# Optimization experiments

Measured on AMD Instinct MI355X. Metric: run time of the kernel, lower is better.

## Reference

```python
import jax, jax.numpy as jnp
import numpy as np

B, T, D = 4, 2048, 1024
F = 4 * D  # Config.RWKV_INTERMIDATE_SIZE * hidden_dim
LN_EPS = 1e-3  # keras LayerNormalization default epsilon


def layer_norm(x, g, b, eps=LN_EPS):
    mu = jnp.mean(x, axis=-1, keepdims=True)
    var = jnp.mean(jnp.square(x - mu), axis=-1, keepdims=True)
    return (x - mu) * jax.lax.rsqrt(var + eps) * g + b


def setup_inputs() -> dict:
    ks = jax.random.split(jax.random.key(0), 24)
    g = lambda k, shape: (jax.random.normal(k, shape, jnp.float32)
                          * np.sqrt(2.0 / sum(shape)))  # ~glorot
    return {
        "x": jax.random.normal(ks[0], (B, T, D), jnp.float32),
        "s_cm": jnp.zeros((B, D), jnp.float32),
        "s_tm": jnp.zeros((B, D), jnp.float32),
        "s_num": jnp.zeros((B, D), jnp.float32),
        "s_den": jnp.zeros((B, D), jnp.float32),
        "s_q": jnp.zeros((B, D), jnp.float32),
        "ln1_g": jnp.ones((D,), jnp.float32),
        "ln1_b": jnp.zeros((D,), jnp.float32),
        "ln2_g": jnp.ones((D,), jnp.float32),
        "ln2_b": jnp.zeros((D,), jnp.float32),
        "tm_mix_k": jax.random.uniform(ks[1], (D,), jnp.float32, 0.0, 2.0 / D),
        "tm_mix_v": jax.random.uniform(ks[2], (D,), jnp.float32, 0.0, 2.0 / D),
        "tm_mix_r": jax.random.uniform(ks[3], (D,), jnp.float32, 0.0, (2.0 / D) ** 0.5),
        "tm_kw": g(ks[4], (D, D)),
        "tm_vw": g(ks[5], (D, D)),
        "tm_rw": g(ks[6], (D, D)),
        "time_decay": jax.random.uniform(ks[7], (D,), jnp.float32, 0.0, 0.1),
        "time_first": jax.random.uniform(ks[8], (D,), jnp.float32, 0.0, 0.05),
        "out_w": g(ks[9], (D, D)),
        "cm_mix_k": jax.random.uniform(ks[10], (D,), jnp.float32, 0.0, 2.0 / D),
        "cm_mix_r": jax.random.uniform(ks[11], (D,), jnp.float32, 0.0, 2.0 / D),
        "cm_kw": g(ks[12], (D, F)),
        "cm_vw": g(ks[13], (F, D)),
        "cm_rw": g(ks[14], (D, D)),
    }


def _shift(h, s):
    # token shift: prepend last-token state, drop last timestep
    return jnp.concatenate([s[:, None, :], h[:, :-1, :]], axis=1)


def reference(x, s_cm, s_tm, s_num, s_den, s_q,
              ln1_g, ln1_b, ln2_g, ln2_b,
              tm_mix_k, tm_mix_v, tm_mix_r, tm_kw, tm_vw, tm_rw,
              time_decay, time_first, out_w,
              cm_mix_k, cm_mix_r, cm_kw, cm_vw, cm_rw):
    # ---- time mixing ----
    h = layer_norm(x, ln1_g, ln1_b)  # [B,T,D]
    hs = _shift(h, s_tm)
    xk = h * tm_mix_k + hs * (1.0 - tm_mix_k)
    xv = h * tm_mix_v + hs * (1.0 - tm_mix_v)
    xr = h * tm_mix_r + hs * (1.0 - tm_mix_r)
    k = xk @ tm_kw  # [B,T,D]
    v = xv @ tm_vw
    r = jax.nn.sigmoid(xr @ tm_rw)
    w = -jnp.exp(time_decay)  # [D]

    def step(carry, kv):
        num, den, q = carry
        kt, vt = kv  # [B,D]
        mo = jnp.maximum(q, kt + time_first)
        e1 = jnp.exp(q - mo)
        e2 = jnp.exp(kt + time_first - mo)
        out = (e1 * num + e2 * vt) / (e1 * den + e2)
        ms = jnp.maximum(q + w, kt)
        e1s = jnp.exp(q + w - ms)
        e2s = jnp.exp(kt - ms)
        return (e1s * num + e2s * vt, e1s * den + e2s, ms), out

    (num, den, q), wkv = jax.lax.scan(
        step, (s_num, s_den, s_q),
        (k.transpose(1, 0, 2), v.transpose(1, 0, 2)))
    wkv = wkv.transpose(1, 0, 2)  # [B,T,D]
    x = x + (r * wkv) @ out_w

    # ---- channel mixing ----
    h2 = layer_norm(x, ln2_g, ln2_b)
    hs2 = _shift(h2, s_cm)
    xk2 = h2 * cm_mix_k + hs2 * (1.0 - cm_mix_k)
    xr2 = h2 * cm_mix_r + hs2 * (1.0 - cm_mix_r)
    kv = jnp.square(jax.nn.relu(xk2 @ cm_kw)) @ cm_vw  # [B,T,F] -> [B,T,D]
    x = x + jax.nn.sigmoid(xr2 @ cm_rw) * kv

    # new state: (cm_inputs, tm_inputs, num, den, q)
    return x, h2[:, -1], h[:, -1], num, den, q
```

## Files before the change

kernel.cpp:

```cpp
#include <hip/hip_runtime.h>

typedef unsigned short ushort_t;
typedef __attribute__((ext_vector_type(8))) short short8;
typedef __attribute__((ext_vector_type(4))) float f32x4;

#define B_ 4
#define T_ 2048
#define D_ 1024
#define F_ 4096
#define M_ (B_*T_)
#define CH_ 64
#define NC_ (T_/CH_)

#define AS1 __attribute__((address_space(1)))
#define AS3 __attribute__((address_space(3)))

__device__ __forceinline__ ushort_t f2bf(float f) {
  union { float f; unsigned u; } a; a.f = f;
  unsigned r = a.u + 0x7FFFu + ((a.u >> 16) & 1u);
  return (ushort_t)(r >> 16);
}

__device__ __forceinline__ void gl_lds16(const void* g, void* l) {
  __builtin_amdgcn_global_load_lds((AS1 void*)(__UINTPTR_TYPE__)g,
                                   (AS3 void*)l, 16, 0, 0);
}

__global__ __launch_bounds__(256) void tconv(const float* __restrict__ W,
                                             ushort_t* __restrict__ Wt,
                                             int K, int N) {
  __shared__ float tile[32][33];
  int tx = threadIdx.x, ty = threadIdx.y;
  int n0 = blockIdx.x * 32, k0 = blockIdx.y * 32;
  #pragma unroll
  for (int i = 0; i < 32; i += 8)
    tile[ty + i][tx] = W[(size_t)(k0 + ty + i) * N + n0 + tx];
  __syncthreads();
  #pragma unroll
  for (int i = 0; i < 32; i += 8)
    Wt[(size_t)(n0 + ty + i) * K + k0 + tx] = f2bf(tile[tx][ty + i]);
}

__global__ __launch_bounds__(256) void tconv5(const float* __restrict__ s0,
                                              const float* __restrict__ s1,
                                              const float* __restrict__ s2,
                                              const float* __restrict__ s3,
                                              const float* __restrict__ s4,
                                              ushort_t* __restrict__ d0,
                                              ushort_t* __restrict__ d1,
                                              ushort_t* __restrict__ d2,
                                              ushort_t* __restrict__ d3,
                                              ushort_t* __restrict__ d4) {
  __shared__ float tile[32][33];
  int z = blockIdx.z;
  const float* W = (z == 0) ? s0 : (z == 1) ? s1 : (z == 2) ? s2 : (z == 3) ? s3 : s4;
  ushort_t* Wt   = (z == 0) ? d0 : (z == 1) ? d1 : (z == 2) ? d2 : (z == 3) ? d3 : d4;
  int tx = threadIdx.x, ty = threadIdx.y;
  int n0 = blockIdx.x * 32, k0 = blockIdx.y * 32;
  #pragma unroll
  for (int i = 0; i < 32; i += 8)
    tile[ty + i][tx] = W[(size_t)(k0 + ty + i) * D_ + n0 + tx];
  __syncthreads();
  #pragma unroll
  for (int i = 0; i < 32; i += 8)
    Wt[(size_t)(n0 + ty + i) * D_ + k0 + tx] = f2bf(tile[tx][ty + i]);
}

#define MIX1(c, p, f) f2bf((c) * (f) + (p) * (1.0f - (f)))

template <int NOUT>
__global__ __launch_bounds__(256)
void ln_mix(const float* __restrict__ xin, const float* __restrict__ st,
            const float* __restrict__ g, const float* __restrict__ bb,
            const float* __restrict__ mk, const float* __restrict__ mv,
            const float* __restrict__ mr,
            ushort_t* __restrict__ ok, ushort_t* __restrict__ ov,
            ushort_t* __restrict__ orr, float* __restrict__ last) {
  int row = blockIdx.x;
  int t = row & (T_ - 1);
  int b = row >> 11;
  int tid = threadIdx.x;
  const bool pln = (t != 0);
  float4 vc = ((const float4*)(xin + (size_t)row * D_))[tid];
  float4 vp = pln ? ((const float4*)(xin + (size_t)(row - 1) * D_))[tid]
                  : ((const float4*)(st + (size_t)b * D_))[tid];
  float s0 = vc.x + vc.y + vc.z + vc.w;
  float s1 = vc.x * vc.x + vc.y * vc.y + vc.z * vc.z + vc.w * vc.w;
  float s2 = vp.x + vp.y + vp.z + vp.w;
  float s3 = vp.x * vp.x + vp.y * vp.y + vp.z * vp.z + vp.w * vp.w;
  #pragma unroll
  for (int o = 32; o > 0; o >>= 1) {
    s0 += __shfl_down(s0, o); s1 += __shfl_down(s1, o);
    s2 += __shfl_down(s2, o); s3 += __shfl_down(s3, o);
  }
  __shared__ float red[4][4];
  if ((tid & 63) == 0) {
    int w = tid >> 6;
    red[w][0] = s0; red[w][1] = s1; red[w][2] = s2; red[w][3] = s3;
  }
  __syncthreads();
  float cs0 = red[0][0] + red[1][0] + red[2][0] + red[3][0];
  float cs1 = red[0][1] + red[1][1] + red[2][1] + red[3][1];
  float ps0 = red[0][2] + red[1][2] + red[2][2] + red[3][2];
  float ps1 = red[0][3] + red[1][3] + red[2][3] + red[3][3];

  float mu = cs0 * (1.0f / D_);
  float rs = rsqrtf(cs1 * (1.0f / D_) - mu * mu + 1e-3f);
  float4 gv = ((const float4*)g)[tid];
  float4 bv = ((const float4*)bb)[tid];
  float hc[4], hp[4];
  hc[0] = (vc.x - mu) * rs * gv.x + bv.x;
  hc[1] = (vc.y - mu) * rs * gv.y + bv.y;
  hc[2] = (vc.z - mu) * rs * gv.z + bv.z;
  hc[3] = (vc.w - mu) * rs * gv.w + bv.w;
  if (pln) {
    float mup = ps0 * (1.0f / D_);
    float rsp = rsqrtf(ps1 * (1.0f / D_) - mup * mup + 1e-3f);
    hp[0] = (vp.x - mup) * rsp * gv.x + bv.x;
    hp[1] = (vp.y - mup) * rsp * gv.y + bv.y;
    hp[2] = (vp.z - mup) * rsp * gv.z + bv.z;
    hp[3] = (vp.w - mup) * rsp * gv.w + bv.w;
  } else {
    hp[0] = vp.x; hp[1] = vp.y; hp[2] = vp.z; hp[3] = vp.w;
  }

  size_t qi = (size_t)row * 256 + tid;
  float4 k4 = ((const float4*)mk)[tid];
  float4 r4 = ((const float4*)mr)[tid];
  ushort4 o4;
  o4.x = MIX1(hc[0], hp[0], k4.x); o4.y = MIX1(hc[1], hp[1], k4.y);
  o4.z = MIX1(hc[2], hp[2], k4.z); o4.w = MIX1(hc[3], hp[3], k4.w);
  ((ushort4*)ok)[qi] = o4;
  if (NOUT == 3) {
    float4 v4 = ((const float4*)mv)[tid];
    o4.x = MIX1(hc[0], hp[0], v4.x); o4.y = MIX1(hc[1], hp[1], v4.y);
    o4.z = MIX1(hc[2], hp[2], v4.z); o4.w = MIX1(hc[3], hp[3], v4.w);
    ((ushort4*)ov)[qi] = o4;
  }
  o4.x = MIX1(hc[0], hp[0], r4.x); o4.y = MIX1(hc[1], hp[1], r4.y);
  o4.z = MIX1(hc[2], hp[2], r4.z); o4.w = MIX1(hc[3], hp[3], r4.w);
  ((ushort4*)orr)[qi] = o4;

  if (t == T_ - 1) {
    float4 h4; h4.x = hc[0]; h4.y = hc[1]; h4.z = hc[2]; h4.w = hc[3];
    ((float4*)(last + (size_t)b * D_))[tid] = h4;
  }
}

__global__ __launch_bounds__(256) void wkv_part1(const float* __restrict__ k,
                                                 const float* __restrict__ v,
                                                 const float* __restrict__ tdec,
                                                 float* __restrict__ cn,
                                                 float* __restrict__ cd,
                                                 float* __restrict__ cq) {
  int idx = blockIdx.x * 256 + threadIdx.x;
  int d = idx & (D_ - 1);
  int b = (idx >> 10) & (B_ - 1);
  int c = idx >> 12;
  float w = -__expf(tdec[d]);
  const float* kp = k + ((size_t)b * T_ + c * CH_) * D_ + d;
  const float* vp = v + ((size_t)b * T_ + c * CH_) * D_ + d;
  float num = 0.0f, den = 0.0f, q = -1e30f;
  for (int t0 = 0; t0 < CH_; t0 += 8) {
    float kt[8], vt[8];
    #pragma unroll
    for (int i = 0; i < 8; ++i) {
      size_t off = (size_t)(t0 + i) * D_;
      kt[i] = kp[off]; vt[i] = vp[off];
    }
    #pragma unroll
    for (int i = 0; i < 8; ++i) {
      float kk = kt[i];
      float ms = fmaxf(q + w, kk);
      float e1 = __expf(q + w - ms), e2 = __expf(kk - ms);
      num = e1 * num + e2 * vt[i];
      den = e1 * den + e2;
      q = ms;
    }
  }
  cn[idx] = num; cd[idx] = den; cq[idx] = q;
}

__global__ __launch_bounds__(256) void wkv_part2(const float* __restrict__ cn,
                                                 const float* __restrict__ cd,
                                                 const float* __restrict__ cq,
                                                 const float* __restrict__ sn,
                                                 const float* __restrict__ sd,
                                                 const float* __restrict__ sq,
                                                 const float* __restrict__ tdec,
                                                 float* __restrict__ pn,
                                                 float* __restrict__ pd,
                                                 float* __restrict__ pq,
                                                 float* __restrict__ on,
                                                 float* __restrict__ od,
                                                 float* __restrict__ oq) {
  int idx = blockIdx.x * 256 + threadIdx.x;
  int d = idx & (D_ - 1);
  float w = -__expf(tdec[d]);
  float wL = w * (float)CH_;
  float num = sn[idx], den = sd[idx], q = sq[idx];
  #pragma unroll 4
  for (int c = 0; c < NC_; ++c) {
    int j = (c << 12) + idx;
    pn[j] = num; pd[j] = den; pq[j] = q;
    float m2 = cq[j];
    float qn = fmaxf(q + wL, m2);
    float e1 = __expf(q + wL - qn), e2 = __expf(m2 - qn);
    num = e1 * num + e2 * cn[j];
    den = e1 * den + e2 * cd[j];
    q = qn;
  }
  on[idx] = num; od[idx] = den; oq[idx] = q;
}

__global__ __launch_bounds__(256) void wkv_part3(const float* __restrict__ k,
                                                 const float* __restrict__ v,
                                                 const float* __restrict__ r,
                                                 const float* __restrict__ pn,
                                                 const float* __restrict__ pd,
                                                 const float* __restrict__ pq,
                                                 const float* __restrict__ tdec,
                                                 const float* __restrict__ tfirst,
                                                 ushort_t* __restrict__ rwkv) {
  int idx = blockIdx.x * 256 + threadIdx.x;
  int d = idx & (D_ - 1);
  int b = (idx >> 10) & (B_ - 1);
  int c = idx >> 12;
  float w = -__expf(tdec[d]);
  float tf = tfirst[d];
  float num = pn[idx], den = pd[idx], q = pq[idx];
  size_t base = ((size_t)b * T_ + c * CH_) * D_ + d;
  const float* kp = k + base;
  const float* vp = v + base;
  const float* rp = r + base;
  ushort_t* op = rwkv + base;
  for (int t0 = 0; t0 < CH_; t0 += 8) {
    float kt[8], vt[8], rt[8];
    #pragma unroll
    for (int i = 0; i < 8; ++i) {
      size_t off = (size_t)(t0 + i) * D_;
      kt[i] = kp[off]; vt[i] = vp[off]; rt[i] = rp[off];
    }
    #pragma unroll
    for (int i = 0; i < 8; ++i) {
      float kk = kt[i];
      float mo = fmaxf(q, kk + tf);
      float e1 = __expf(q - mo), e2 = __expf(kk + tf - mo);
      float o = (e1 * num + e2 * vt[i]) / (e1 * den + e2);
      op[(size_t)(t0 + i) * D_] = f2bf(rt[i] * o);
      float ms = fmaxf(q + w, kk);
      float e1s = __expf(q + w - ms), e2s = __expf(kk - ms);
      num = e1s * num + e2s * vt[i];
      den = e1s * den + e2s;
      q = ms;
    }
  }
}

template <int EPI>
__global__ __launch_bounds__(512, 2)
void gemm256(const ushort_t* __restrict__ A, const ushort_t* __restrict__ Bt,
             int N, int K, int ktn,
             float* __restrict__ Cf, float* __restrict__ Cf2,
             ushort_t* __restrict__ Cb) {
  __shared__ alignas(16) ushort_t sA[2][256 * 64];
  __shared__ alignas(16) ushort_t sB[2][256 * 64];
  const int tid = threadIdx.x;
  const int lane = tid & 63;
  const int wave = tid >> 6;
  const int wr = wave >> 2, wc = wave & 3;
  const int l15 = lane & 15;
  const int kb = (lane >> 4) << 4;
  const int m0 = blockIdx.x * 256, n0 = blockIdx.y * 256;
  const int kt0 = (EPI == 0) ? blockIdx.z * ktn : 0;
  const ushort_t* gA = A + (size_t)m0 * K + (size_t)kt0 * 64;
  const ushort_t* gB = Bt + (size_t)n0 * K + (size_t)kt0 * 64;

  const int sr = tid >> 3;
  const int sc8 = (tid & 7) ^ (sr & 7);
  const int scb = (tid & 7) * 16;

  auto stage = [&](int dbuf, int kt, int h) {
    const ushort_t* g = (h < 2) ? gA : gB;
    ushort_t* sb = (h < 2) ? sA[dbuf] : sB[dbuf];
    int rbase = (h & 1) * 128;
    #pragma unroll
    for (int i = 0; i < 2; ++i) {
      int row = rbase + i * 64 + sr;
      gl_lds16(g + (size_t)row * K + (size_t)kt * 64 + sc8 * 8,
               (char*)sb + row * 128 + scb);
    }
  };

  auto ld = [&](const ushort_t* sbuf, int row, int s5) -> short8 {
    int cb = ((s5 << 6) + kb) ^ ((row & 7) << 4);
    return *(const short8*)((const char*)sbuf + row * 128 + cb);
  };

  f32x4 acc[8][4] = {};

  stage(0, 0, 0); stage(0, 0, 1); stage(0, 0, 2); stage(0, 0, 3);

  for (int t = 0; t < ktn; ++t) {
    const int cur = t & 1, nxt = cur ^ 1;
    const bool more = (t + 1 < ktn);
    if (more) { stage(nxt, t + 1, 0); stage(nxt, t + 1, 1); }
    if (more) asm volatile("s_waitcnt vmcnt(4)" ::: "memory");
    else      asm volatile("s_waitcnt vmcnt(0)" ::: "memory");
    __builtin_amdgcn_s_barrier();

    const ushort_t* curA = sA[cur];
    const ushort_t* curB = sB[cur];
    short8 bfr[4][2];

#define G256_MFMA16(MI0, A00, A01, A10, A11)                                  \
    __builtin_amdgcn_s_setprio(1);                                            \
    _Pragma("unroll")                                                         \
    for (int ni = 0; ni < 4; ++ni) {                                          \
      acc[MI0][ni] = __builtin_amdgcn_mfma_f32_16x16x32_bf16(                 \
          A00, bfr[ni][0], acc[MI0][ni], 0, 0, 0);                            \
      acc[MI0][ni] = __builtin_amdgcn_mfma_f32_16x16x32_bf16(                 \
          A01, bfr[ni][1], acc[MI0][ni], 0, 0, 0);                            \
      acc[MI0 + 1][ni] = __builtin_amdgcn_mfma_f32_16x16x32_bf16(             \
          A10, bfr[ni][0], acc[MI0 + 1][ni], 0, 0, 0);                        \
      acc[MI0 + 1][ni] = __builtin_amdgcn_mfma_f32_16x16x32_bf16(             \
          A11, bfr[ni][1], acc[MI0 + 1][ni], 0, 0, 0);                        \
    }                                                                         \
    __builtin_amdgcn_s_setprio(0);

#define G256_SYNC_IN()                                                        \
    asm volatile("" ::: "memory");                                            \
    __builtin_amdgcn_s_barrier();                                             \
    asm volatile("s_waitcnt lgkmcnt(0)" ::: "memory");                        \
    __builtin_amdgcn_sched_barrier(0);

#define G256_SYNC_OUT()                                                       \
    asm volatile("" ::: "memory");                                            \
    __builtin_amdgcn_s_barrier();

    {
      #pragma unroll
      for (int ni = 0; ni < 4; ++ni)
        #pragma unroll
        for (int s = 0; s < 2; ++s)
          bfr[ni][s] = ld(curB, wc * 64 + ni * 16 + l15, s);
      short8 a00 = ld(curA, wr * 128 + 0 * 16 + l15, 0);
      short8 a01 = ld(curA, wr * 128 + 0 * 16 + l15, 1);
      short8 a10 = ld(curA, wr * 128 + 1 * 16 + l15, 0);
      short8 a11 = ld(curA, wr * 128 + 1 * 16 + l15, 1);
      if (more) stage(nxt, t + 1, 2);
      G256_SYNC_IN();
      G256_MFMA16(0, a00, a01, a10, a11);
      G256_SYNC_OUT();
    }
    {
      short8 a00 = ld(curA, wr * 128 + 2 * 16 + l15, 0);
      short8 a01 = ld(curA, wr * 128 + 2 * 16 + l15, 1);
      short8 a10 = ld(curA, wr * 128 + 3 * 16 + l15, 0);
      short8 a11 = ld(curA, wr * 128 + 3 * 16 + l15, 1);
      if (more) stage(nxt, t + 1, 3);
      G256_SYNC_IN();
      G256_MFMA16(2, a00, a01, a10, a11);
      G256_SYNC_OUT();
    }
    {
      short8 a00 = ld(curA, wr * 128 + 4 * 16 + l15, 0);
      short8 a01 = ld(curA, wr * 128 + 4 * 16 + l15, 1);
      short8 a10 = ld(curA, wr * 128 + 5 * 16 + l15, 0);
      short8 a11 = ld(curA, wr * 128 + 5 * 16 + l15, 1);
      G256_SYNC_IN();
      G256_MFMA16(4, a00, a01, a10, a11);
      G256_SYNC_OUT();
    }
    {
      short8 a00 = ld(curA, wr * 128 + 6 * 16 + l15, 0);
      short8 a01 = ld(curA, wr * 128 + 6 * 16 + l15, 1);
      short8 a10 = ld(curA, wr * 128 + 7 * 16 + l15, 0);
      short8 a11 = ld(curA, wr * 128 + 7 * 16 + l15, 1);
      G256_SYNC_IN();
      G256_MFMA16(6, a00, a01, a10, a11);
      G256_SYNC_OUT();
    }
  }

  float* cfp = (EPI == 0 && blockIdx.z) ? Cf2 : Cf;
  #pragma unroll
  for (int mi = 0; mi < 8; ++mi)
    #pragma unroll
    for (int ni = 0; ni < 4; ++ni)
      #pragma unroll
      for (int j = 0; j < 4; ++j) {
        int row = m0 + wr * 128 + mi * 16 + ((lane >> 4) << 2) + j;
        int col = n0 + wc * 64 + ni * 16 + l15;
        size_t idx = (size_t)row * N + col;
        float v = acc[mi][ni][j];
        if (EPI == 0) {
          cfp[idx] = v;
        } else {
          float tt = v > 0.0f ? v : 0.0f;
          Cb[idx] = f2bf(tt * tt);
        }
      }
}

template <int EPI>
__global__ __launch_bounds__(512, 2)
void gemmB(const ushort_t* __restrict__ A, const ushort_t* __restrict__ Bt,
           int K, int ktn,
           float* __restrict__ Cf, float* __restrict__ Cf2,
           float* __restrict__ Cf3,
           const float* __restrict__ X, const float* __restrict__ X2) {
  __shared__ alignas(16) ushort_t sA[2][128 * 64];
  __shared__ alignas(16) ushort_t sB[2][256 * 64];
  const int tid = threadIdx.x;
  const int lane = tid & 63;
  const int wave = tid >> 6;
  const int wr = wave >> 2, wc = wave & 3;
  const int l15 = lane & 15;
  const int kb = (lane >> 4) << 4;
  const int m0 = blockIdx.x * 128, n0 = blockIdx.y * 256;
  const int zid = blockIdx.z;

  const ushort_t* Ause = A;
  const ushort_t* Buse = Bt;
  if (EPI == 3) {
    Ause = A + (size_t)zid * M_ * D_;
    Buse = Bt + (size_t)zid * D_ * D_;
  }
  const ushort_t* gA = Ause + (size_t)m0 * K;
  const ushort_t* gB = Buse + (size_t)n0 * K;

  const int sr = tid >> 3;
  const int sc8 = (tid & 7) ^ (sr & 7);
  const int scb = (tid & 7) * 16;

  auto stage = [&](int dbuf, int kt, int h) {
    if (h < 2) {
      int row = h * 64 + sr;
      gl_lds16(gA + (size_t)row * K + (size_t)kt * 64 + sc8 * 8,
               (char*)sA[dbuf] + row * 128 + scb);
    } else {
      int rbase = (h - 2) * 128;
      #pragma unroll
      for (int i = 0; i < 2; ++i) {
        int row = rbase + i * 64 + sr;
        gl_lds16(gB + (size_t)row * K + (size_t)kt * 64 + sc8 * 8,
                 (char*)sB[dbuf] + row * 128 + scb);
      }
    }
  };

  auto ld = [&](const ushort_t* sbuf, int row, int s5) -> short8 {
    int cb = ((s5 << 6) + kb) ^ ((row & 7) << 4);
    return *(const short8*)((const char*)sbuf + row * 128 + cb);
  };

  f32x4 acc[4][4] = {};

  stage(0, 0, 0); stage(0, 0, 1); stage(0, 0, 2); stage(0, 0, 3);

  for (int t = 0; t < ktn; ++t) {
    const int cur = t & 1, nxt = cur ^ 1;
    const bool more = (t + 1 < ktn);
    if (more) {
      stage(nxt, t + 1, 0); stage(nxt, t + 1, 1);
      stage(nxt, t + 1, 2); stage(nxt, t + 1, 3);
    }
    if (more) asm volatile("s_waitcnt vmcnt(6)" ::: "memory");
    else      asm volatile("s_waitcnt vmcnt(0)" ::: "memory");
    __builtin_amdgcn_s_barrier();

    const ushort_t* curA = sA[cur];
    const ushort_t* curB = sB[cur];

    #pragma unroll
    for (int s = 0; s < 2; ++s) {
      short8 av[4], bv[4];
      #pragma unroll
      for (int i = 0; i < 4; ++i) av[i] = ld(curA, wr * 64 + i * 16 + l15, s);
      #pragma unroll
      for (int i = 0; i < 4; ++i) bv[i] = ld(curB, wc * 64 + i * 16 + l15, s);
      asm volatile("" ::: "memory");
      __builtin_amdgcn_s_barrier();
      asm volatile("s_waitcnt lgkmcnt(0)" ::: "memory");
      __builtin_amdgcn_sched_barrier(0);
      __builtin_amdgcn_s_setprio(1);
      #pragma unroll
      for (int mi = 0; mi < 4; ++mi)
        #pragma unroll
        for (int ni = 0; ni < 4; ++ni)
          acc[mi][ni] = __builtin_amdgcn_mfma_f32_16x16x32_bf16(
              av[mi], bv[ni], acc[mi][ni], 0, 0, 0);
      __builtin_amdgcn_s_setprio(0);
      asm volatile("" ::: "memory");
      __builtin_amdgcn_s_barrier();
    }
  }

  float* dst = Cf;
  if (EPI == 3) dst = (zid == 0) ? Cf : (zid == 1 ? Cf2 : Cf3);
  #pragma unroll
  for (int mi = 0; mi < 4; ++mi)
    #pragma unroll
    for (int ni = 0; ni < 4; ++ni)
      #pragma unroll
      for (int j = 0; j < 4; ++j) {
        int row = m0 + wr * 64 + mi * 16 + ((lane >> 4) << 2) + j;
        int col = n0 + wc * 64 + ni * 16 + l15;
        size_t idx = (size_t)row * D_ + col;
        float v = acc[mi][ni][j];
        if (EPI == 2) {
          dst[idx] = X[idx] + v;
        } else if (EPI == 3) {
          dst[idx] = (zid == 2) ? 1.0f / (1.0f + __expf(-v)) : v;
        } else if (EPI == 4) {
          float s = 1.0f / (1.0f + __expf(-v));
          dst[idx] = X2[idx] + s * (X[idx] + Cf3[idx]);
        }
      }
}

extern "C" void kernel_launch(void* const* d_in, const int* in_sizes, int n_in,
                              void* d_out, int out_size, void* d_ws, size_t ws_size,
                              hipStream_t stream) {
  const float* x      = (const float*)d_in[0];
  const float* s_cm   = (const float*)d_in[1];
  const float* s_tm   = (const float*)d_in[2];
  const float* s_num  = (const float*)d_in[3];
  const float* s_den  = (const float*)d_in[4];
  const float* s_q    = (const float*)d_in[5];
  const float* ln1_g  = (const float*)d_in[6];
  const float* ln1_b  = (const float*)d_in[7];
  const float* ln2_g  = (const float*)d_in[8];
  const float* ln2_b  = (const float*)d_in[9];
  const float* tmk    = (const float*)d_in[10];
  const float* tmv    = (const float*)d_in[11];
  const float* tmr    = (const float*)d_in[12];
  const float* tm_kw  = (const float*)d_in[13];
  const float* tm_vw  = (const float*)d_in[14];
  const float* tm_rw  = (const float*)d_in[15];
  const float* tdec   = (const float*)d_in[16];
  const float* tfirst = (const float*)d_in[17];
  const float* out_w  = (const float*)d_in[18];
  const float* cmk    = (const float*)d_in[19];
  const float* cmr    = (const float*)d_in[20];
  const float* cm_kw  = (const float*)d_in[21];
  const float* cm_vw  = (const float*)d_in[22];
  const float* cm_rw  = (const float*)d_in[23];

  float* out   = (float*)d_out;
  float* o_x   = out;
  float* o_h2l = out + (size_t)M_ * D_;
  float* o_hl  = o_h2l + B_ * D_;
  float* o_num = o_hl + B_ * D_;
  float* o_den = o_num + B_ * D_;
  float* o_q   = o_den + B_ * D_;

  char* W = (char*)d_ws;
  const size_t MB = 1024 * 1024;
  ushort_t* w_tmk = (ushort_t*)(W + 0 * MB);
  ushort_t* w_tmv = (ushort_t*)(W + 2 * MB);
  ushort_t* w_tmr = (ushort_t*)(W + 4 * MB);
  ushort_t* w_out = (ushort_t*)(W + 6 * MB);
  ushort_t* w_cmk = (ushort_t*)(W + 8 * MB);
  ushort_t* w_cmv = (ushort_t*)(W + 16 * MB);
  ushort_t* w_cmr = (ushort_t*)(W + 24 * MB);
  float*    hbuf  = (float*)(W + 26 * MB);
  ushort_t* xk    = (ushort_t*)(W + 58 * MB);
  ushort_t* xv    = (ushort_t*)(W + 74 * MB);
  ushort_t* xr    = (ushort_t*)(W + 90 * MB);
  float*    kbuf  = (float*)(W + 106 * MB);
  float*    vbuf  = (float*)(W + 138 * MB);
  float*    rbuf  = (float*)(W + 170 * MB);
  ushort_t* rwkv  = xr;
  ushort_t* xk2   = xk;
  ushort_t* xr2   = xv;
  ushort_t* kk    = (ushort_t*)kbuf;
  float*    kv_a  = rbuf;
  float*    kv_b  = hbuf;

  float* cn = (float*)(W + 26 * MB + 0 * 512 * 1024);
  float* cd = (float*)(W + 26 * MB + 1 * 512 * 1024);
  float* cq = (float*)(W + 26 * MB + 2 * 512 * 1024);
  float* pn = (float*)(W + 26 * MB + 3 * 512 * 1024);
  float* pd = (float*)(W + 26 * MB + 4 * 512 * 1024);
  float* pq = (float*)(W + 26 * MB + 5 * 512 * 1024);

  dim3 tb(32, 8);
  tconv5<<<dim3(D_/32, D_/32, 5), tb, 0, stream>>>(tm_kw, tm_vw, tm_rw, out_w, cm_rw,
                                                   w_tmk, w_tmv, w_tmr, w_out, w_cmr);
  tconv<<<dim3(F_/32, D_/32), tb, 0, stream>>>(cm_kw, w_cmk, D_, F_);
  tconv<<<dim3(D_/32, F_/32), tb, 0, stream>>>(cm_vw, w_cmv, F_, D_);

  ln_mix<3><<<M_, 256, 0, stream>>>(x, s_tm, ln1_g, ln1_b, tmk, tmv, tmr,
                                    xk, xv, xr, o_hl);
  gemmB<3><<<dim3(M_/128, D_/256, 3), 512, 0, stream>>>(
      xk, w_tmk, D_, D_/64, kbuf, vbuf, rbuf, nullptr, nullptr);

  wkv_part1<<<(NC_ * B_ * D_) / 256, 256, 0, stream>>>(kbuf, vbuf, tdec, cn, cd, cq);
  wkv_part2<<<(B_ * D_) / 256, 256, 0, stream>>>(cn, cd, cq, s_num, s_den, s_q, tdec,
                                                 pn, pd, pq, o_num, o_den, o_q);
  wkv_part3<<<(NC_ * B_ * D_) / 256, 256, 0, stream>>>(kbuf, vbuf, rbuf, pn, pd, pq,
                                                       tdec, tfirst, rwkv);

  gemmB<2><<<dim3(M_/128, D_/256, 1), 512, 0, stream>>>(
      rwkv, w_out, D_, D_/64, o_x, nullptr, nullptr, x, nullptr);

  ln_mix<2><<<M_, 256, 0, stream>>>(o_x, s_cm, ln2_g, ln2_b, cmk, nullptr, cmr,
                                    xk2, nullptr, xr2, o_h2l);
  gemm256<1><<<dim3(M_/256, F_/256, 1), 512, 0, stream>>>(
      xk2, w_cmk, F_, D_, D_/64, nullptr, nullptr, kk);
  gemm256<0><<<dim3(M_/256, D_/256, 2), 512, 0, stream>>>(
      kk, w_cmv, D_, F_, F_/128, kv_a, kv_b, nullptr);
  gemmB<4><<<dim3(M_/128, D_/256, 1), 512, 0, stream>>>(
      xr2, w_cmr, D_, D_/64, o_x, nullptr, kv_b, kv_a, o_x);
}
```

Measured before the change: 432.2 us.

## Store k/v/r in bf16, add XCD block swizzle, drop split-K for down-projection

The k/v/r projection outputs are now written as bf16 instead of fp32, and the WKV scan kernels read and convert them, which halves that intermediate traffic. Blocks in gemm256 and gemmB are remapped with an XCD-aware swizzle so that neighbouring tiles land on the same chiplet and share L2. The split-K gemm256<0> for the F->D projection, with its two partial fp32 outputs, is replaced by a single gemmB<5> over the full K, which removes the extra partial-sum read in the final epilogue. The cost is reduced precision for k/v/r feeding the exp-based recurrence, and the unsplit GEMM launches fewer blocks.

```diff
diff --git a/kernel.cpp b/kernel.cpp
--- a/kernel.cpp
+++ b/kernel.cpp
@@ -21,9 +21,25 @@
   return (ushort_t)(r >> 16);
 }
 
+__device__ __forceinline__ float bf2f(ushort_t u) {
+  union { unsigned u; float f; } a; a.u = ((unsigned)u) << 16;
+  return a.f;
+}
+
 __device__ __forceinline__ void gl_lds16(const void* g, void* l) {
   __builtin_amdgcn_global_load_lds((AS1 void*)(__UINTPTR_TYPE__)g,
                                    (AS3 void*)l, 16, 0, 0);
+}
+
+__device__ __forceinline__ void xcd_swz(int gx, int gy, int& bx, int& by, int& bz) {
+  int lid = blockIdx.x + gx * (blockIdx.y + gy * blockIdx.z);
+  int nwg = gx * gy * gridDim.z;
+  int cpx = nwg >> 3;
+  int L = (lid & 7) * cpx + (lid >> 3);
+  by = L % gy;
+  int t1 = L / gy;
+  bx = t1 % gx;
+  bz = t1 / gx;
 }
 
 __global__ __launch_bounds__(256) void tconv(const float* __restrict__ W,
@@ -147,8 +163,8 @@
   }
 }
 
-__global__ __launch_bounds__(256) void wkv_part1(const float* __restrict__ k,
-                                                 const float* __restrict__ v,
+__global__ __launch_bounds__(256) void wkv_part1(const ushort_t* __restrict__ k,
+                                                 const ushort_t* __restrict__ v,
                                                  const float* __restrict__ tdec,
                                                  float* __restrict__ cn,
                                                  float* __restrict__ cd,
@@ -158,15 +174,15 @@
   int b = (idx >> 10) & (B_ - 1);
   int c = idx >> 12;
   float w = -__expf(tdec[d]);
-  const float* kp = k + ((size_t)b * T_ + c * CH_) * D_ + d;
-  const float* vp = v + ((size_t)b * T_ + c * CH_) * D_ + d;
+  const ushort_t* kp = k + ((size_t)b * T_ + c * CH_) * D_ + d;
+  const ushort_t* vp = v + ((size_t)b * T_ + c * CH_) * D_ + d;
   float num = 0.0f, den = 0.0f, q = -1e30f;
   for (int t0 = 0; t0 < CH_; t0 += 8) {
     float kt[8], vt[8];
     #pragma unroll
     for (int i = 0; i < 8; ++i) {
       size_t off = (size_t)(t0 + i) * D_;
-      kt[i] = kp[off]; vt[i] = vp[off];
+      kt[i] = bf2f(kp[off]); vt[i] = bf2f(vp[off]);
     }
     #pragma unroll
     for (int i = 0; i < 8; ++i) {
@@ -213,9 +229,9 @@
   on[idx] = num; od[idx] = den; oq[idx] = q;
 }
 
-__global__ __launch_bounds__(256) void wkv_part3(const float* __restrict__ k,
-                                                 const float* __restrict__ v,
-                                                 const float* __restrict__ r,
+__global__ __launch_bounds__(256) void wkv_part3(const ushort_t* __restrict__ k,
+                                                 const ushort_t* __restrict__ v,
+                                                 const ushort_t* __restrict__ r,
                                                  const float* __restrict__ pn,
                                                  const float* __restrict__ pd,
                                                  const float* __restrict__ pq,
@@ -230,16 +246,16 @@
   float tf = tfirst[d];
   float num = pn[idx], den = pd[idx], q = pq[idx];
   size_t base = ((size_t)b * T_ + c * CH_) * D_ + d;
-  const float* kp = k + base;
-  const float* vp = v + base;
-  const float* rp = r + base;
+  const ushort_t* kp = k + base;
+  const ushort_t* vp = v + base;
+  const ushort_t* rp = r + base;
   ushort_t* op = rwkv + base;
   for (int t0 = 0; t0 < CH_; t0 += 8) {
     float kt[8], vt[8], rt[8];
     #pragma unroll
     for (int i = 0; i < 8; ++i) {
       size_t off = (size_t)(t0 + i) * D_;
-      kt[i] = kp[off]; vt[i] = vp[off]; rt[i] = rp[off];
+      kt[i] = bf2f(kp[off]); vt[i] = bf2f(vp[off]); rt[i] = bf2f(rp[off]);
     }
     #pragma unroll
     for (int i = 0; i < 8; ++i) {
@@ -260,9 +276,7 @@
 template <int EPI>
 __global__ __launch_bounds__(512, 2)
 void gemm256(const ushort_t* __restrict__ A, const ushort_t* __restrict__ Bt,
-             int N, int K, int ktn,
-             float* __restrict__ Cf, float* __restrict__ Cf2,
-             ushort_t* __restrict__ Cb) {
+             int N, int K, int ktn, ushort_t* __restrict__ Cb) {
   __shared__ alignas(16) ushort_t sA[2][256 * 64];
   __shared__ alignas(16) ushort_t sB[2][256 * 64];
   const int tid = threadIdx.x;
@@ -271,10 +285,11 @@
   const int wr = wave >> 2, wc = wave & 3;
   const int l15 = lane & 15;
   const int kb = (lane >> 4) << 4;
-  const int m0 = blockIdx.x * 256, n0 = blockIdx.y * 256;
-  const int kt0 = (EPI == 0) ? blockIdx.z * ktn : 0;
-  const ushort_t* gA = A + (size_t)m0 * K + (size_t)kt0 * 64;
-  const ushort_t* gB = Bt + (size_t)n0 * K + (size_t)kt0 * 64;
+  int bx, by, bz;
+  xcd_swz(gridDim.x, gridDim.y, bx, by, bz);
+  const int m0 = bx * 256, n0 = by * 256;
+  const ushort_t* gA = A + (size_t)m0 * K;
+  const ushort_t* gB = Bt + (size_t)n0 * K;
 
   const int sr = tid >> 3;
   const int sc8 = (tid & 7) ^ (sr & 7);
@@ -383,7 +398,6 @@
     }
   }
 
-  float* cfp = (EPI == 0 && blockIdx.z) ? Cf2 : Cf;
   #pragma unroll
   for (int mi = 0; mi < 8; ++mi)
     #pragma unroll
@@ -394,12 +408,8 @@
         int col = n0 + wc * 64 + ni * 16 + l15;
         size_t idx = (size_t)row * N + col;
         float v = acc[mi][ni][j];
-        if (EPI == 0) {
-          cfp[idx] = v;
-        } else {
-          float tt = v > 0.0f ? v : 0.0f;
-          Cb[idx] = f2bf(tt * tt);
-        }
+        float tt = v > 0.0f ? v : 0.0f;
+        Cb[idx] = f2bf(tt * tt);
       }
 }
 
@@ -407,8 +417,7 @@
 __global__ __launch_bounds__(512, 2)
 void gemmB(const ushort_t* __restrict__ A, const ushort_t* __restrict__ Bt,
            int K, int ktn,
-           float* __restrict__ Cf, float* __restrict__ Cf2,
-           float* __restrict__ Cf3,
+           float* __restrict__ Cf, ushort_t* __restrict__ Ub,
            const float* __restrict__ X, const float* __restrict__ X2) {
   __shared__ alignas(16) ushort_t sA[2][128 * 64];
   __shared__ alignas(16) ushort_t sB[2][256 * 64];
@@ -418,8 +427,9 @@
   const int wr = wave >> 2, wc = wave & 3;
   const int l15 = lane & 15;
   const int kb = (lane >> 4) << 4;
-  const int m0 = blockIdx.x * 128, n0 = blockIdx.y * 256;
-  const int zid = blockIdx.z;
+  int bx, by, zid;
+  xcd_swz(gridDim.x, gridDim.y, bx, by, zid);
+  const int m0 = bx * 128, n0 = by * 256;
 
   const ushort_t* Ause = A;
   const ushort_t* Buse = Bt;
@@ -497,8 +507,7 @@
     }
   }
 
-  float* dst = Cf;
-  if (EPI == 3) dst = (zid == 0) ? Cf : (zid == 1 ? Cf2 : Cf3);
+  ushort_t* ub = (EPI == 3) ? Ub + (size_t)zid * M_ * D_ : nullptr;
   #pragma unroll
   for (int mi = 0; mi < 4; ++mi)
     #pragma unroll
@@ -510,12 +519,15 @@
         size_t idx = (size_t)row * D_ + col;
         float v = acc[mi][ni][j];
         if (EPI == 2) {
-          dst[idx] = X[idx] + v;
+          Cf[idx] = X[idx] + v;
         } else if (EPI == 3) {
-          dst[idx] = (zid == 2) ? 1.0f / (1.0f + __expf(-v)) : v;
+          if (zid == 2) v = 1.0f / (1.0f + __expf(-v));
+          ub[idx] = f2bf(v);
         } else if (EPI == 4) {
           float s = 1.0f / (1.0f + __expf(-v));
-          dst[idx] = X2[idx] + s * (X[idx] + Cf3[idx]);
+          Cf[idx] = X2[idx] + s * X[idx];
+        } else if (EPI == 5) {
+          Cf[idx] = v;
         }
       }
 }
@@ -565,26 +577,23 @@
   ushort_t* w_cmk = (ushort_t*)(W + 8 * MB);
   ushort_t* w_cmv = (ushort_t*)(W + 16 * MB);
   ushort_t* w_cmr = (ushort_t*)(W + 24 * MB);
-  float*    hbuf  = (float*)(W + 26 * MB);
-  ushort_t* xk    = (ushort_t*)(W + 58 * MB);
-  ushort_t* xv    = (ushort_t*)(W + 74 * MB);
-  ushort_t* xr    = (ushort_t*)(W + 90 * MB);
-  float*    kbuf  = (float*)(W + 106 * MB);
-  float*    vbuf  = (float*)(W + 138 * MB);
-  float*    rbuf  = (float*)(W + 170 * MB);
-  ushort_t* rwkv  = xr;
-  ushort_t* xk2   = xk;
-  ushort_t* xr2   = xv;
-  ushort_t* kk    = (ushort_t*)kbuf;
-  float*    kv_a  = rbuf;
-  float*    kv_b  = hbuf;
-
   float* cn = (float*)(W + 26 * MB + 0 * 512 * 1024);
   float* cd = (float*)(W + 26 * MB + 1 * 512 * 1024);
   float* cq = (float*)(W + 26 * MB + 2 * 512 * 1024);
   float* pn = (float*)(W + 26 * MB + 3 * 512 * 1024);
   float* pd = (float*)(W + 26 * MB + 4 * 512 * 1024);
   float* pq = (float*)(W + 26 * MB + 5 * 512 * 1024);
+  ushort_t* xk    = (ushort_t*)(W + 32 * MB);
+  ushort_t* xv    = (ushort_t*)(W + 48 * MB);
+  ushort_t* xr    = (ushort_t*)(W + 64 * MB);
+  ushort_t* kbuf  = (ushort_t*)(W + 80 * MB);
+  ushort_t* vbuf  = (ushort_t*)(W + 96 * MB);
+  ushort_t* rbuf  = (ushort_t*)(W + 112 * MB);
+  ushort_t* kk    = (ushort_t*)(W + 128 * MB);
+  float*    kv    = (float*)(W + 80 * MB);
+  ushort_t* rwkv  = xr;
+  ushort_t* xk2   = xk;
+  ushort_t* xr2   = xv;
 
   dim3 tb(32, 8);
   tconv5<<<dim3(D_/32, D_/32, 5), tb, 0, stream>>>(tm_kw, tm_vw, tm_rw, out_w, cm_rw,
@@ -595,7 +604,7 @@
   ln_mix<3><<<M_, 256, 0, stream>>>(x, s_tm, ln1_g, ln1_b, tmk, tmv, tmr,
                                     xk, xv, xr, o_hl);
   gemmB<3><<<dim3(M_/128, D_/256, 3), 512, 0, stream>>>(
-      xk, w_tmk, D_, D_/64, kbuf, vbuf, rbuf, nullptr, nullptr);
+      xk, w_tmk, D_, D_/64, nullptr, kbuf, nullptr, nullptr);
 
   wkv_part1<<<(NC_ * B_ * D_) / 256, 256, 0, stream>>>(kbuf, vbuf, tdec, cn, cd, cq);
   wkv_part2<<<(B_ * D_) / 256, 256, 0, stream>>>(cn, cd, cq, s_num, s_den, s_q, tdec,
@@ -604,14 +613,14 @@
                                                        tdec, tfirst, rwkv);
 
   gemmB<2><<<dim3(M_/128, D_/256, 1), 512, 0, stream>>>(
-      rwkv, w_out, D_, D_/64, o_x, nullptr, nullptr, x, nullptr);
+      rwkv, w_out, D_, D_/64, o_x, nullptr, x, nullptr);
 
   ln_mix<2><<<M_, 256, 0, stream>>>(o_x, s_cm, ln2_g, ln2_b, cmk, nullptr, cmr,
                                     xk2, nullptr, xr2, o_h2l);
   gemm256<1><<<dim3(M_/256, F_/256, 1), 512, 0, stream>>>(
-      xk2, w_cmk, F_, D_, D_/64, nullptr, nullptr, kk);
-  gemm256<0><<<dim3(M_/256, D_/256, 2), 512, 0, stream>>>(
-      kk, w_cmv, D_, F_, F_/128, kv_a, kv_b, nullptr);
+      xk2, w_cmk, F_, D_, D_/64, kk);
+  gemmB<5><<<dim3(M_/128, D_/256, 1), 512, 0, stream>>>(
+      kk, w_cmv, F_, F_/64, kv, nullptr, nullptr, nullptr);
   gemmB<4><<<dim3(M_/128, D_/256, 1), 512, 0, stream>>>(
-      xr2, w_cmr, D_, D_/64, o_x, nullptr, kv_b, kv_a, o_x);
-}
+      xr2, w_cmr, D_, D_/64, o_x, nullptr, kv, o_x);
+}
```

After: 429.0 us. Within noise of the previous version (-0.7%).
